# Kernel tuning notes

Measured on AMD Instinct MI355X. Metric: run time of the kernel, lower is better.

Reference implementation:

```python
import jax, jax.numpy as jnp
import numpy as np

T, N, C, RADIUS = 64, 16, 256, 64
D_OUT = 2 * RADIUS + 1
TAU = 2.0
DECAY = float(np.exp(-1.0 / TAU))  # first-order leaky (LIF) filter decay
WEIGHT0 = 6.53543197272069


def setup_inputs() -> dict:
    key = jax.random.key(0)
    k1, k2 = jax.random.split(key)
    inp = jax.random.uniform(k1, (T, N, C, 2), dtype=jnp.float32)
    delay_param = jnp.arange(-RADIUS, RADIUS + 1, dtype=jnp.float32)[:, None]  # (D_out, 1)
    weight = jnp.asarray(WEIGHT0, dtype=jnp.float32)
    u = jax.random.uniform(k2, (N, C, D_OUT, 2), dtype=jnp.float32)  # bernoulli uniforms
    return {"input": inp, "delay_param": delay_param, "weight": weight, "u": u}


def reference(input, delay_param, weight, u):
    Tn, Nn, Cn, _ = input.shape
    # delay = relu(cat([_delay, -_delay], dim=1))  -> (D_out, 2), nonnegative
    delay = jax.nn.relu(jnp.concatenate([delay_param, -delay_param], axis=1))
    Do = delay.shape[0]
    # input.unsqueeze(-2).repeat(..., D_out, 1) -> (T, N, C, D_out, 2)
    x = jnp.broadcast_to(input[:, :, :, None, :], (Tn, Nn, Cn, Do, 2))
    # stochastic rounding of per-synapse delay
    bd = jnp.broadcast_to(delay[None, None], (Nn, Cn, Do, 2))
    df = jnp.floor(bd)
    rounded = jnp.where(u < bd - df, df + 1.0, df)
    # clamp so the (one-hot) spike at argmax(t) stays inside the window
    spike_t = jnp.argmax(x, axis=0)  # (N, C, D_out, 2)
    rounded = jnp.minimum(rounded, (Tn - 1 - spike_t).astype(rounded.dtype))
    d = rounded.astype(jnp.int32)
    # circular shift along time: out[t] = x[(t - d) % T]
    t_idx = jnp.arange(Tn)[:, None, None, None, None]
    idx = (t_idx - d[None]) % Tn
    shifted = jnp.take_along_axis(x, idx, axis=0)  # (T, N, C, D_out, 2)
    # LIF filter (leaky integrator over time, state reset at t=0)
    def step(v, xt):
        v = v * DECAY + xt
        return v, v
    _, filt = jax.lax.scan(step, jnp.zeros_like(shifted[0]), shifted)
    # scale by fixed synaptic weight and sum over the 2 input channels
    return jnp.sum(filt * weight, axis=-1)  # (T, N, C, D_out)
```

## Files before the change

kernel.cpp:

```cpp
#include <hip/hip_runtime.h>

#define T_DIM 64
#define NP 4096
#define D_OUTC 129
#define ROW_STRIDE (NP * D_OUTC)

__global__ __launch_bounds__(128, 8) void jeffress_kernel(
    const float* __restrict__ input,
    const float* __restrict__ delay_param,
    const float* __restrict__ weight,
    const float* __restrict__ u,
    float* __restrict__ out)
{
    __shared__ float Hw0[128], Hw1[128];
    __shared__ int caps[2];

    const int p    = ((blockIdx.x & 7) << 9) | (blockIdx.x >> 3);
    const int tid  = threadIdx.x;
    const int lane = tid & 63, wv = tid >> 6;
    const float DECAY = 0.6065306597126334f;

    float2 xp = ((const float2*)input)[lane * NP + p];

    {
        float xv = wv ? xp.y : xp.x;
        unsigned b = __float_as_uint(xv);
        b ^= (b & 0x80000000u) ? 0xffffffffu : 0x80000000u;
        unsigned long long key = ((unsigned long long)b << 32) | (unsigned)(63 - lane);
        #pragma unroll
        for (int mm = 1; mm < 64; mm <<= 1) {
            unsigned long long o = __shfl_xor(key, mm, 64);
            if (o > key) key = o;
        }
        if (lane == 0) caps[wv] = (int)(key & 0xffffffffull);
    }

    const float w = weight[0];
    if (wv == 0) {
        float v0 = xp.x, v1 = xp.y;
        const float dks[6] = {0.6065306597126334f,
                              0.36787944117144233f,
                              0.1353352832366127f,
                              0.01831563888873418f,
                              3.3546262790251185e-4f,
                              1.1253517471925912e-7f};
        #pragma unroll
        for (int k = 0; k < 6; ++k) {
            int o = 1 << k;
            float p0 = __shfl_up(v0, o, 64);
            float p1 = __shfl_up(v1, o, 64);
            if (lane >= o) { v0 += dks[k] * p0; v1 += dks[k] * p1; }
        }
        Hw0[lane] = w * v0;
        Hw1[lane] = w * v1;
    }
    __syncthreads();
    if (wv == 1) {
        float f = exp2f(-0.7213475204444817f * (float)(lane + 1));
        Hw0[64 + lane] = Hw0[lane] + f * Hw0[63];
        Hw1[64 + lane] = Hw1[lane] + f * Hw1[63];
    }
    __syncthreads();

    const float c0f = (float)caps[0], c1f = (float)caps[1];

    auto calc = [&](int dd, int& s0, int& s1) {
        float dp = delay_param[dd];
        float b0 = fmaxf(dp, 0.0f), b1 = fmaxf(-dp, 0.0f);
        float2 uu = ((const float2*)u)[p * D_OUTC + dd];
        float f0 = floorf(b0), f1 = floorf(b1);
        float r0 = (uu.x < b0 - f0) ? f0 + 1.0f : f0;
        float r1 = (uu.y < b1 - f1) ? f1 + 1.0f : f1;
        s0 = (int)fminf(r0, c0f);
        s1 = (int)fminf(r1, c1f);
    };

    int s0, s1; calc(tid, s0, s1);
    const float* pA0 = &Hw0[64 - s0];
    const float* pA1 = &Hw1[64 - s1];
    const float Cw = pA0[-1] + pA1[-1];

    const bool dual = (tid == 127);
    int e0 = 0, e1 = 0; if (dual) calc(128, e0, e1);
    const float* pB0 = &Hw0[64 - e0];
    const float* pB1 = &Hw1[64 - e1];
    const float CwE = dual ? (pB0[-1] + pB1[-1]) : 0.0f;

    float* rp = out + (size_t)p * D_OUTC + tid;
    float Dg = DECAY;
    const float K[8] = {1.0f, 0.6065306597126334f, 0.36787944117144233f,
                        0.22313016014842982f, 0.1353352832366127f,
                        0.0820849986238988f, 0.049787068367863944f,
                        0.030197383422318501f};

    for (int tg = 0; tg < T_DIM; tg += 8) {
        float CwD  = Cw  * Dg;
        float CwDE = CwE * Dg;
        #pragma unroll
        for (int j = 0; j < 8; ++j) {
            float val = pA0[tg + j] + pA1[tg + j] - K[j] * CwD;
            rp[0] = val;
            if (dual) {
                float ve = pB0[tg + j] + pB1[tg + j] - K[j] * CwDE;
                rp[1] = ve;
            }
            rp += ROW_STRIDE;
        }
        Dg *= 0.01831563888873418f;
    }
}

extern "C" void kernel_launch(void* const* d_in, const int* in_sizes, int n_in,
                              void* d_out, int out_size, void* d_ws, size_t ws_size,
                              hipStream_t stream) {
    const float* input       = (const float*)d_in[0];
    const float* delay_param = (const float*)d_in[1];
    const float* weight      = (const float*)d_in[2];
    const float* u           = (const float*)d_in[3];
    float* out = (float*)d_out;

    jeffress_kernel<<<NP, 128, 0, stream>>>(input, delay_param, weight, u, out);
}
```

Measured before the change: 162.7 us.

## Process four positions per block with wave-local prefix scans and 8-byte stores

Each 256-thread block now handles four (n,c) positions, with one wave per position computing both channels' argmax and the LIF prefix scan. The second-half scan extension is done with a shuffle instead of a second barrier phase. Each thread then writes two adjacent outputs per time step as a float2 over a contiguous 516-element row segment. The aim is fewer blocks, fewer barriers and wider, better-coalesced stores. In exchange, per-thread shared-memory indexing is more complex and some stores fall on unaligned 8-byte addresses.

Result: faster. 157.1 us (-3.5%).

```diff
diff --git a/kernel.cpp b/kernel.cpp
--- a/kernel.cpp
+++ b/kernel.cpp
@@ -4,39 +4,43 @@
 #define NP 4096
 #define D_OUTC 129
 #define ROW_STRIDE (NP * D_OUTC)
+#define PPB 4
 
-__global__ __launch_bounds__(128, 8) void jeffress_kernel(
+typedef float v2f __attribute__((ext_vector_type(2)));
+
+__global__ __launch_bounds__(256, 4) void jeffress_kernel(
     const float* __restrict__ input,
     const float* __restrict__ delay_param,
     const float* __restrict__ weight,
     const float* __restrict__ u,
     float* __restrict__ out)
 {
-    __shared__ float Hw0[128], Hw1[128];
-    __shared__ int caps[2];
+    __shared__ float Hw[PPB * 2 * 128];
+    __shared__ int caps[PPB][2];
 
-    const int p    = ((blockIdx.x & 7) << 9) | (blockIdx.x >> 3);
-    const int tid  = threadIdx.x;
+    const int blk = blockIdx.x;
+    const int g   = ((blk & 7) << 7) | (blk >> 3);
+    const int p0  = g * PPB;
+    const int tid = threadIdx.x;
     const int lane = tid & 63, wv = tid >> 6;
     const float DECAY = 0.6065306597126334f;
-
-    float2 xp = ((const float2*)input)[lane * NP + p];
+    const float w = weight[0];
 
     {
-        float xv = wv ? xp.y : xp.x;
-        unsigned b = __float_as_uint(xv);
-        b ^= (b & 0x80000000u) ? 0xffffffffu : 0x80000000u;
-        unsigned long long key = ((unsigned long long)b << 32) | (unsigned)(63 - lane);
+        float2 xp = ((const float2*)input)[lane * NP + p0 + wv];
         #pragma unroll
-        for (int mm = 1; mm < 64; mm <<= 1) {
-            unsigned long long o = __shfl_xor(key, mm, 64);
-            if (o > key) key = o;
+        for (int ch = 0; ch < 2; ++ch) {
+            float xv = ch ? xp.y : xp.x;
+            unsigned b = __float_as_uint(xv);
+            b ^= (b & 0x80000000u) ? 0xffffffffu : 0x80000000u;
+            unsigned long long key = ((unsigned long long)b << 32) | (unsigned)(63 - lane);
+            #pragma unroll
+            for (int mm = 1; mm < 64; mm <<= 1) {
+                unsigned long long o = __shfl_xor(key, mm, 64);
+                if (o > key) key = o;
+            }
+            if (lane == 0) caps[wv][ch] = (int)(key & 0xffffffffull);
         }
-        if (lane == 0) caps[wv] = (int)(key & 0xffffffffull);
-    }
-
-    const float w = weight[0];
-    if (wv == 0) {
         float v0 = xp.x, v1 = xp.y;
         const float dks[6] = {0.6065306597126334f,
                               0.36787944117144233f,
@@ -47,64 +51,71 @@
         #pragma unroll
         for (int k = 0; k < 6; ++k) {
             int o = 1 << k;
-            float p0 = __shfl_up(v0, o, 64);
-            float p1 = __shfl_up(v1, o, 64);
-            if (lane >= o) { v0 += dks[k] * p0; v1 += dks[k] * p1; }
+            float q0 = __shfl_up(v0, o, 64);
+            float q1 = __shfl_up(v1, o, 64);
+            if (lane >= o) { v0 += dks[k] * q0; v1 += dks[k] * q1; }
         }
-        Hw0[lane] = w * v0;
-        Hw1[lane] = w * v1;
-    }
-    __syncthreads();
-    if (wv == 1) {
+        float h063 = __shfl(v0, 63, 64);
+        float h163 = __shfl(v1, 63, 64);
         float f = exp2f(-0.7213475204444817f * (float)(lane + 1));
-        Hw0[64 + lane] = Hw0[lane] + f * Hw0[63];
-        Hw1[64 + lane] = Hw1[lane] + f * Hw1[63];
+        float* H0 = &Hw[(wv * 2 + 0) * 128];
+        float* H1 = &Hw[(wv * 2 + 1) * 128];
+        H0[lane] = w * v0;  H0[64 + lane] = w * (v0 + f * h063);
+        H1[lane] = w * v1;  H1[64 + lane] = w * (v1 + f * h163);
     }
     __syncthreads();
 
-    const float c0f = (float)caps[0], c1f = (float)caps[1];
-
-    auto calc = [&](int dd, int& s0, int& s1) {
-        float dp = delay_param[dd];
+    auto mke = [&](int q, int& o0, int& o1, float& Cw) {
+        int pl = q / 129;
+        int d  = q - 129 * pl;
+        float dp = delay_param[d];
         float b0 = fmaxf(dp, 0.0f), b1 = fmaxf(-dp, 0.0f);
-        float2 uu = ((const float2*)u)[p * D_OUTC + dd];
+        float2 uu = ((const float2*)u)[(p0 + pl) * D_OUTC + d];
         float f0 = floorf(b0), f1 = floorf(b1);
         float r0 = (uu.x < b0 - f0) ? f0 + 1.0f : f0;
         float r1 = (uu.y < b1 - f1) ? f1 + 1.0f : f1;
-        s0 = (int)fminf(r0, c0f);
-        s1 = (int)fminf(r1, c1f);
+        int s0 = (int)fminf(r0, (float)caps[pl][0]);
+        int s1 = (int)fminf(r1, (float)caps[pl][1]);
+        o0 = (pl * 2 + 0) * 128 + 64 - s0;
+        o1 = (pl * 2 + 1) * 128 + 64 - s1;
+        Cw = Hw[o0 - 1] + Hw[o1 - 1];
     };
 
-    int s0, s1; calc(tid, s0, s1);
-    const float* pA0 = &Hw0[64 - s0];
-    const float* pA1 = &Hw1[64 - s1];
-    const float Cw = pA0[-1] + pA1[-1];
+    int oA0, oA1, oB0, oB1; float CwA, CwB;
+    mke(2 * tid,     oA0, oA1, CwA);
+    mke(2 * tid + 1, oB0, oB1, CwB);
+    const bool xtra = (tid < 2);
+    int oC0 = 0, oC1 = 0, oD0 = 0, oD1 = 0; float CwC = 0.0f, CwDd = 0.0f;
+    if (xtra) {
+        mke(512 + 2 * tid, oC0, oC1, CwC);
+        mke(513 + 2 * tid, oD0, oD1, CwDd);
+    }
 
-    const bool dual = (tid == 127);
-    int e0 = 0, e1 = 0; if (dual) calc(128, e0, e1);
-    const float* pB0 = &Hw0[64 - e0];
-    const float* pB1 = &Hw1[64 - e1];
-    const float CwE = dual ? (pB0[-1] + pB1[-1]) : 0.0f;
+    float* rp  = out + (size_t)p0 * D_OUTC + 2 * tid;
+    float* rpx = out + (size_t)p0 * D_OUTC + 512 + 2 * tid;
 
-    float* rp = out + (size_t)p * D_OUTC + tid;
-    float Dg = DECAY;
     const float K[8] = {1.0f, 0.6065306597126334f, 0.36787944117144233f,
                         0.22313016014842982f, 0.1353352832366127f,
                         0.0820849986238988f, 0.049787068367863944f,
                         0.030197383422318501f};
+    float Dg = DECAY;
 
     for (int tg = 0; tg < T_DIM; tg += 8) {
-        float CwD  = Cw  * Dg;
-        float CwDE = CwE * Dg;
+        float cA = CwA * Dg, cB = CwB * Dg;
+        float cC = CwC * Dg, cD = CwDd * Dg;
         #pragma unroll
         for (int j = 0; j < 8; ++j) {
-            float val = pA0[tg + j] + pA1[tg + j] - K[j] * CwD;
-            rp[0] = val;
-            if (dual) {
-                float ve = pB0[tg + j] + pB1[tg + j] - K[j] * CwDE;
-                rp[1] = ve;
+            int t = tg + j;
+            v2f v;
+            v.x = Hw[oA0 + t] + Hw[oA1 + t] - K[j] * cA;
+            v.y = Hw[oB0 + t] + Hw[oB1 + t] - K[j] * cB;
+            *(v2f*)(rp + (size_t)t * ROW_STRIDE) = v;
+            if (xtra) {
+                v2f vx;
+                vx.x = Hw[oC0 + t] + Hw[oC1 + t] - K[j] * cC;
+                vx.y = Hw[oD0 + t] + Hw[oD1 + t] - K[j] * cD;
+                *(v2f*)(rpx + (size_t)t * ROW_STRIDE) = vx;
             }
-            rp += ROW_STRIDE;
         }
         Dg *= 0.01831563888873418f;
     }
@@ -119,5 +130,5 @@
     const float* u           = (const float*)d_in[3];
     float* out = (float*)d_out;
 
-    jeffress_kernel<<<NP, 128, 0, stream>>>(input, delay_param, weight, u, out);
+    jeffress_kernel<<<NP / PPB, 256, 0, stream>>>(input, delay_param, weight, u, out);
 }
```
